# Performance work log

Hardware: AMD Instinct MI355X
Metric: run time of the kernel (lower is better)

The kernel has to match this reference:

```python
import jax, jax.numpy as jnp
import numpy as np

H_OBJ, W_OBJ = 64, 64  # must match init_kwargs object_shape


def setup_inputs() -> dict:
    key = jax.random.key(0)
    k1, k2 = jax.random.split(key)
    image = jax.random.normal(k1, (512, 3, 256, 256), dtype=jnp.float32)
    # y, x, height, width in (0.1, 1): keeps theta invertible (torch code asserts no NaN)
    z_where = jax.random.uniform(k2, (512, 4), dtype=jnp.float32, minval=0.1, maxval=1.0)
    return {"image": image, "z_where": z_where, "inverse": 1}


def _build_theta(z_where, inverse):
    y, x, h, w = jnp.split(z_where, 4, axis=-1)  # each [N,1]
    y = y * 2.0 - 1.0
    x = x * 2.0 - 1.0
    y, x, h, w = y[:, 0], x[:, 0], h[:, 0], w[:, 0]
    zero = jnp.zeros_like(w)
    if inverse:
        # theta is [[w,0,x],[0,h,y],[0,0,1]]; closed-form inverse (== torch .inverse())
        row0 = jnp.stack([1.0 / w, zero, -x / w], axis=-1)
        row1 = jnp.stack([zero, 1.0 / h, -y / h], axis=-1)
    else:
        row0 = jnp.stack([w, zero, x], axis=-1)
        row1 = jnp.stack([zero, h, y], axis=-1)
    return jnp.stack([row0, row1], axis=-2)  # [N,2,3]


def _affine_grid(theta, H_out, W_out):
    # align_corners=True normalized coords
    xs = jnp.linspace(-1.0, 1.0, W_out, dtype=theta.dtype)
    ys = jnp.linspace(-1.0, 1.0, H_out, dtype=theta.dtype)
    gx, gy = jnp.meshgrid(xs, ys)  # [H_out, W_out]
    base = jnp.stack([gx, gy, jnp.ones_like(gx)], axis=-1)  # [H,W,3]
    return jnp.einsum('nij,hwj->nhwi', theta, base)  # [N,H,W,2] -> (x, y)


def _grid_sample_border(image, grid):
    # bilinear, padding_mode='border', align_corners=True
    N, C, Hin, Win = image.shape
    ix = (grid[..., 0] + 1.0) * 0.5 * (Win - 1)  # [N,Ho,Wo]
    iy = (grid[..., 1] + 1.0) * 0.5 * (Hin - 1)
    ix = jnp.clip(ix, 0.0, Win - 1)
    iy = jnp.clip(iy, 0.0, Hin - 1)
    ix0f = jnp.floor(ix)
    iy0f = jnp.floor(iy)
    wx = ix - ix0f
    wy = iy - iy0f
    ix0 = jnp.clip(ix0f.astype(jnp.int32), 0, Win - 1)
    iy0 = jnp.clip(iy0f.astype(jnp.int32), 0, Hin - 1)
    ix1 = jnp.clip(ix0 + 1, 0, Win - 1)
    iy1 = jnp.clip(iy0 + 1, 0, Hin - 1)

    def gather(img, yi, xi):
        return img[:, yi, xi]  # [C,Ho,Wo]

    g = jax.vmap(gather)
    v00 = g(image, iy0, ix0)
    v01 = g(image, iy0, ix1)
    v10 = g(image, iy1, ix0)
    v11 = g(image, iy1, ix1)
    wx = wx[:, None]  # [N,1,Ho,Wo]
    wy = wy[:, None]
    return (v00 * (1 - wx) * (1 - wy) + v01 * wx * (1 - wy)
            + v10 * (1 - wx) * wy + v11 * wx * wy)


def reference(image, z_where, inverse):
    theta = _build_theta(z_where, inverse)
    grid = _affine_grid(theta, H_OBJ, W_OBJ)
    glimpse = _grid_sample_border(image, grid)  # [N,C,H_OBJ,W_OBJ]
    return glimpse.reshape(glimpse.shape[0], -1)
```

## Files before the change

kernel.cpp:

```cpp
#include <hip/hip_runtime.h>

#define H_OBJ 64
#define W_OBJ 64
#define HIN 256
#define WIN 256
#define NCH 3

__global__ __launch_bounds__(256) void stn_glimpse_kernel(
    const float* __restrict__ image,
    const float* __restrict__ zwhere,
    const int* __restrict__ inv_p,
    float* __restrict__ out)
{
    const int n   = blockIdx.x >> 4;
    const int pix = ((blockIdx.x & 15) << 8) + threadIdx.x;
    const int i   = pix >> 6;
    const int j   = pix & 63;

    const float zy = zwhere[n * 4 + 0];
    const float zx = zwhere[n * 4 + 1];
    const float zh = zwhere[n * 4 + 2];
    const float zw = zwhere[n * 4 + 3];
    const float y  = zy * 2.0f - 1.0f;
    const float x  = zx * 2.0f - 1.0f;

    const float gx = -1.0f + (2.0f / 63.0f) * (float)j;
    const float gy = -1.0f + (2.0f / 63.0f) * (float)i;

    const int inv = *inv_p;
    float grid_x, grid_y;
    if (inv) {
        grid_x = (gx - x) / zw;
        grid_y = (gy - y) / zh;
    } else {
        grid_x = zw * gx + x;
        grid_y = zh * gy + y;
    }

    float ix = (grid_x + 1.0f) * 0.5f * (float)(WIN - 1);
    float iy = (grid_y + 1.0f) * 0.5f * (float)(HIN - 1);
    ix = fminf(fmaxf(ix, 0.0f), (float)(WIN - 1));
    iy = fminf(fmaxf(iy, 0.0f), (float)(HIN - 1));

    const float ix0f = floorf(ix);
    const float iy0f = floorf(iy);
    const float wx = ix - ix0f;
    const float wy = iy - iy0f;
    const int ix0 = (int)ix0f;
    const int iy0 = (int)iy0f;
    const int ix1 = min(ix0 + 1, WIN - 1);
    const int iy1 = min(iy0 + 1, HIN - 1);

    const float w00 = (1.0f - wx) * (1.0f - wy);
    const float w01 = wx * (1.0f - wy);
    const float w10 = (1.0f - wx) * wy;
    const float w11 = wx * wy;

    const float* imgN = image + (size_t)n * NCH * HIN * WIN;
    float* outN = out + (size_t)n * NCH * (H_OBJ * W_OBJ) + pix;

    const int o00 = iy0 * WIN + ix0;
    const int o01 = iy0 * WIN + ix1;
    const int o10 = iy1 * WIN + ix0;
    const int o11 = iy1 * WIN + ix1;

#pragma unroll
    for (int c = 0; c < NCH; ++c) {
        const float* ch = imgN + c * (HIN * WIN);
        const float v00 = ch[o00];
        const float v01 = ch[o01];
        const float v10 = ch[o10];
        const float v11 = ch[o11];
        outN[c * (H_OBJ * W_OBJ)] =
            v00 * w00 + v01 * w01 + v10 * w10 + v11 * w11;
    }
}

extern "C" void kernel_launch(void* const* d_in, const int* in_sizes, int n_in,
                              void* d_out, int out_size, void* d_ws, size_t ws_size,
                              hipStream_t stream) {
    const float* image  = (const float*)d_in[0];
    const float* zwhere = (const float*)d_in[1];
    const int*   inv    = (const int*)d_in[2];
    float*       out    = (float*)d_out;

    const int nBatch = in_sizes[1] / 4;
    stn_glimpse_kernel<<<nBatch * 16, 256, 0, stream>>>(image, zwhere, inv, out);
}
```

Before: 24.09 us.

## Remap blocks so each batch image stays on one XCD, two pixels per thread

Measured after the change: 23.78 us. Within noise of the previous version (-1.3%).

```diff
diff --git a/kernel.cpp b/kernel.cpp
--- a/kernel.cpp
+++ b/kernel.cpp
@@ -6,28 +6,16 @@
 #define WIN 256
 #define NCH 3
 
-__global__ __launch_bounds__(256) void stn_glimpse_kernel(
-    const float* __restrict__ image,
-    const float* __restrict__ zwhere,
-    const int* __restrict__ inv_p,
-    float* __restrict__ out)
+__device__ __forceinline__ void sample_pixel(
+    const float* __restrict__ imgN, float* __restrict__ outN,
+    int pix, float x, float y, float zw, float zh, int inv)
 {
-    const int n   = blockIdx.x >> 4;
-    const int pix = ((blockIdx.x & 15) << 8) + threadIdx.x;
-    const int i   = pix >> 6;
-    const int j   = pix & 63;
-
-    const float zy = zwhere[n * 4 + 0];
-    const float zx = zwhere[n * 4 + 1];
-    const float zh = zwhere[n * 4 + 2];
-    const float zw = zwhere[n * 4 + 3];
-    const float y  = zy * 2.0f - 1.0f;
-    const float x  = zx * 2.0f - 1.0f;
+    const int i = pix >> 6;
+    const int j = pix & 63;
 
     const float gx = -1.0f + (2.0f / 63.0f) * (float)j;
     const float gy = -1.0f + (2.0f / 63.0f) * (float)i;
 
-    const int inv = *inv_p;
     float grid_x, grid_y;
     if (inv) {
         grid_x = (gx - x) / zw;
@@ -56,9 +44,6 @@
     const float w10 = (1.0f - wx) * wy;
     const float w11 = wx * wy;
 
-    const float* imgN = image + (size_t)n * NCH * HIN * WIN;
-    float* outN = out + (size_t)n * NCH * (H_OBJ * W_OBJ) + pix;
-
     const int o00 = iy0 * WIN + ix0;
     const int o01 = iy0 * WIN + ix1;
     const int o10 = iy1 * WIN + ix0;
@@ -71,9 +56,46 @@
         const float v01 = ch[o01];
         const float v10 = ch[o10];
         const float v11 = ch[o11];
-        outN[c * (H_OBJ * W_OBJ)] =
-            v00 * w00 + v01 * w01 + v10 * w10 + v11 * w11;
+        __builtin_nontemporal_store(
+            v00 * w00 + v01 * w01 + v10 * w10 + v11 * w11,
+            &outN[c * (H_OBJ * W_OBJ) + pix]);
     }
+}
+
+__global__ __launch_bounds__(256) void stn_glimpse_kernel(
+    const float* __restrict__ image,
+    const float* __restrict__ zwhere,
+    const int* __restrict__ inv_p,
+    float* __restrict__ out,
+    int nBatch, int perXcd)
+{
+    const int s = blockIdx.x;
+    int n, sub;
+    if (perXcd) {
+        const int xcd = s & 7;
+        const int j   = s >> 3;
+        const int bi  = j % perXcd;
+        sub = j / perXcd;
+        n   = xcd + (bi << 3);
+    } else {
+        n   = s >> 3;
+        sub = s & 7;
+    }
+
+    const float zy = zwhere[n * 4 + 0];
+    const float zx = zwhere[n * 4 + 1];
+    const float zh = zwhere[n * 4 + 2];
+    const float zw = zwhere[n * 4 + 3];
+    const float y  = zy * 2.0f - 1.0f;
+    const float x  = zx * 2.0f - 1.0f;
+    const int inv  = *inv_p;
+
+    const float* imgN = image + (size_t)n * NCH * HIN * WIN;
+    float* outN = out + (size_t)n * NCH * (H_OBJ * W_OBJ);
+
+    const int pix0 = (sub << 9) + threadIdx.x;
+    sample_pixel(imgN, outN, pix0,       x, y, zw, zh, inv);
+    sample_pixel(imgN, outN, pix0 + 256, x, y, zw, zh, inv);
 }
 
 extern "C" void kernel_launch(void* const* d_in, const int* in_sizes, int n_in,
@@ -85,5 +107,7 @@
     float*       out    = (float*)d_out;
 
     const int nBatch = in_sizes[1] / 4;
-    stn_glimpse_kernel<<<nBatch * 16, 256, 0, stream>>>(image, zwhere, inv, out);
+    const int perXcd = (nBatch % 8 == 0) ? (nBatch / 8) : 0;
+    stn_glimpse_kernel<<<nBatch * 8, 256, 0, stream>>>(
+        image, zwhere, inv, out, nBatch, perXcd);
 }
```

## Stage needed input rows in LDS with double-buffered coalesced loads

Applied to the files above, without the earlier changes.

After: 60.32 us. +150.3%, slower.

```diff
diff --git a/kernel.cpp b/kernel.cpp
--- a/kernel.cpp
+++ b/kernel.cpp
@@ -5,6 +5,10 @@
 #define HIN 256
 #define WIN 256
 #define NCH 3
+#define G 4
+#define NSLOT (2*G)
+#define ROWS_PER_BLOCK 32
+#define NITER (ROWS_PER_BLOCK/G)
 
 __global__ __launch_bounds__(256) void stn_glimpse_kernel(
     const float* __restrict__ image,
@@ -12,67 +16,98 @@
     const int* __restrict__ inv_p,
     float* __restrict__ out)
 {
-    const int n   = blockIdx.x >> 4;
-    const int pix = ((blockIdx.x & 15) << 8) + threadIdx.x;
-    const int i   = pix >> 6;
-    const int j   = pix & 63;
+    __shared__ float buf[NSLOT][NCH][WIN];
+    float* const bufF = &buf[0][0][0];
 
-    const float zy = zwhere[n * 4 + 0];
-    const float zx = zwhere[n * 4 + 1];
-    const float zh = zwhere[n * 4 + 2];
-    const float zw = zwhere[n * 4 + 3];
-    const float y  = zy * 2.0f - 1.0f;
-    const float x  = zx * 2.0f - 1.0f;
+    const int b    = blockIdx.x;
+    const int n    = b >> 1;
+    const int half = b & 1;
+    const int t    = threadIdx.x;
+    const int j    = t & 63;
+    const int ii   = t >> 6;
 
-    const float gx = -1.0f + (2.0f / 63.0f) * (float)j;
-    const float gy = -1.0f + (2.0f / 63.0f) * (float)i;
+    const float zy = zwhere[n*4+0];
+    const float zx = zwhere[n*4+1];
+    const float zh = zwhere[n*4+2];
+    const float zw = zwhere[n*4+3];
+    const float y  = zy*2.0f - 1.0f;
+    const float x  = zx*2.0f - 1.0f;
+    const float rw = 1.0f/zw;
+    const float rh = 1.0f/zh;
+    const int inv  = *inv_p;
 
-    const int inv = *inv_p;
-    float grid_x, grid_y;
-    if (inv) {
-        grid_x = (gx - x) / zw;
-        grid_y = (gy - y) / zh;
-    } else {
-        grid_x = zw * gx + x;
-        grid_y = zh * gy + y;
-    }
+    const float* imgN = image + (size_t)n * (NCH*HIN*WIN);
+    float* outN = out + (size_t)n * (NCH*H_OBJ*W_OBJ);
 
-    float ix = (grid_x + 1.0f) * 0.5f * (float)(WIN - 1);
-    float iy = (grid_y + 1.0f) * 0.5f * (float)(HIN - 1);
-    ix = fminf(fmaxf(ix, 0.0f), (float)(WIN - 1));
-    iy = fminf(fmaxf(iy, 0.0f), (float)(HIN - 1));
+    const float gx = -1.0f + (2.0f/63.0f)*(float)j;
+    float grid_x = inv ? (gx - x)*rw : (zw*gx + x);
+    float ixf = (grid_x + 1.0f)*0.5f*(float)(WIN-1);
+    ixf = fminf(fmaxf(ixf, 0.0f), (float)(WIN-1));
+    const float ix0f = floorf(ixf);
+    const float wx   = ixf - ix0f;
+    const int ix0    = (int)ix0f;
+    const int xbase  = min(ix0, WIN-2);
+    const bool lo    = (ix0 < WIN-1);
 
-    const float ix0f = floorf(ix);
-    const float iy0f = floorf(iy);
-    const float wx = ix - ix0f;
-    const float wy = iy - iy0f;
-    const int ix0 = (int)ix0f;
-    const int iy0 = (int)iy0f;
-    const int ix1 = min(ix0 + 1, WIN - 1);
-    const int iy1 = min(iy0 + 1, HIN - 1);
+    auto inrow = [&](int i, int par) -> int {
+        const float gy = -1.0f + (2.0f/63.0f)*(float)i;
+        float gyy = inv ? (gy - y)*rh : (zh*gy + y);
+        float iyf = (gyy + 1.0f)*0.5f*(float)(HIN-1);
+        iyf = fminf(fmaxf(iyf, 0.0f), (float)(HIN-1));
+        const int iy0 = (int)floorf(iyf);
+        return par ? min(iy0+1, HIN-1) : iy0;
+    };
 
-    const float w00 = (1.0f - wx) * (1.0f - wy);
-    const float w01 = wx * (1.0f - wy);
-    const float w10 = (1.0f - wx) * wy;
-    const float w11 = wx * wy;
+    auto issue_loads = [&](int k, float4* regs) {
+        const int i0 = half*ROWS_PER_BLOCK + k*G;
+#pragma unroll
+        for (int q = 0; q < 6; ++q) {
+            const int p    = q*4 + ii;
+            const int slot = p/3;
+            const int ch   = p - slot*3;
+            const int row  = inrow(i0 + (slot>>1), slot&1);
+            const float* src = imgN + ch*(HIN*WIN) + row*WIN + 4*j;
+            __builtin_memcpy(&regs[q], src, sizeof(float4));
+        }
+    };
 
-    const float* imgN = image + (size_t)n * NCH * HIN * WIN;
-    float* outN = out + (size_t)n * NCH * (H_OBJ * W_OBJ) + pix;
+    float4 regs[6];
+    issue_loads(0, regs);
 
-    const int o00 = iy0 * WIN + ix0;
-    const int o01 = iy0 * WIN + ix1;
-    const int o10 = iy1 * WIN + ix0;
-    const int o11 = iy1 * WIN + ix1;
+    for (int k = 0; k < NITER; ++k) {
+        __syncthreads();
+#pragma unroll
+        for (int q = 0; q < 6; ++q)
+            reinterpret_cast<float4*>(bufF)[q*256 + t] = regs[q];
+        if (k+1 < NITER) issue_loads(k+1, regs);
+        __syncthreads();
 
+        const int i = half*ROWS_PER_BLOCK + k*G + ii;
+        const float gy = -1.0f + (2.0f/63.0f)*(float)i;
+        float gyy = inv ? (gy - y)*rh : (zh*gy + y);
+        float iyf = (gyy + 1.0f)*0.5f*(float)(HIN-1);
+        iyf = fminf(fmaxf(iyf, 0.0f), (float)(HIN-1));
+        const float wy = iyf - floorf(iyf);
+
+        const float w00 = (1.0f - wx)*(1.0f - wy);
+        const float w01 = wx*(1.0f - wy);
+        const float w10 = (1.0f - wx)*wy;
+        const float w11 = wx*wy;
+
+        const int sT = 2*ii, sB = 2*ii + 1;
 #pragma unroll
-    for (int c = 0; c < NCH; ++c) {
-        const float* ch = imgN + c * (HIN * WIN);
-        const float v00 = ch[o00];
-        const float v01 = ch[o01];
-        const float v10 = ch[o10];
-        const float v11 = ch[o11];
-        outN[c * (H_OBJ * W_OBJ)] =
-            v00 * w00 + v01 * w01 + v10 * w10 + v11 * w11;
+        for (int c = 0; c < NCH; ++c) {
+            float2 top, bot;
+            __builtin_memcpy(&top, &buf[sT][c][xbase], sizeof(float2));
+            __builtin_memcpy(&bot, &buf[sB][c][xbase], sizeof(float2));
+            const float v00 = lo ? top.x : top.y;
+            const float v01 = top.y;
+            const float v10 = lo ? bot.x : bot.y;
+            const float v11 = bot.y;
+            __builtin_nontemporal_store(
+                v00*w00 + v01*w01 + v10*w10 + v11*w11,
+                &outN[c*(H_OBJ*W_OBJ) + i*W_OBJ + j]);
+        }
     }
 }
 
@@ -85,5 +120,5 @@
     float*       out    = (float*)d_out;
 
     const int nBatch = in_sizes[1] / 4;
-    stn_glimpse_kernel<<<nBatch * 16, 256, 0, stream>>>(image, zwhere, inv, out);
+    stn_glimpse_kernel<<<nBatch * 2, 256, 0, stream>>>(image, zwhere, inv, out);
 }
```
